# Performance work log

Hardware: AMD Instinct MI355X
Metric: run time of the kernel (lower is better)

Reference implementation:

```python
import jax, jax.numpy as jnp
import numpy as np

N, D = 8192, 256
NUM_CLASSES = 100
WEIGHT = 1.0


def setup_inputs() -> dict:
    key = jax.random.key(0)
    k1, k2 = jax.random.split(key)
    predictions = jax.random.normal(k1, (N, D), dtype=jnp.float32)
    targets = jax.random.randint(k2, (N,), 0, NUM_CLASSES, dtype=jnp.int32)
    return {"predictions": predictions, "targets": targets}


def reference(predictions, targets):
    # Pairwise squared L2 via ||a||^2 + ||b||^2 - 2 a.b  -> [N, N]
    sq = jnp.sum(predictions * predictions, axis=1)
    d2 = sq[:, None] + sq[None, :] - 2.0 * (predictions @ predictions.T)
    dist = jnp.sqrt(jnp.maximum(d2, 0.0))  # torch.dist(p=2)

    n = predictions.shape[0]
    upper = jnp.triu(jnp.ones((n, n), dtype=bool), k=1)  # i < j pairs only
    same = targets[:, None] == targets[None, :]
    mask = upper & same

    num = jnp.sum(mask).astype(dist.dtype)
    loss = jnp.sum(jnp.where(mask, dist, 0.0)) / num
    return loss * WEIGHT
```

## Files before the change

kernel.cpp:

```cpp
#include <hip/hip_runtime.h>

#define N_CLS 100
#define D_DIM 256
#define MAX_M 112
#define ROW_SH 264
#define PANEL 48
#define HALF_R 56

#define AS1 __attribute__((address_space(1)))
#define AS3 __attribute__((address_space(3)))

typedef short bf16x8 __attribute__((ext_vector_type(8)));
typedef float f32x4  __attribute__((ext_vector_type(4)));

__device__ __forceinline__ unsigned short f2bf(float f) {
    unsigned int b = __float_as_uint(f);
    return (unsigned short)((b + 0x7FFFu + ((b >> 16) & 1u)) >> 16);
}

__device__ __forceinline__ void gl_lds16(const void* g, void* l) {
    __builtin_amdgcn_global_load_lds((AS1 void*)g, (AS3 void*)l, 16, 0, 0);
}

__device__ __forceinline__ void stage(const float* __restrict__ pred,
        const int* bkt, int m, int cp0, int dslot, int cnt,
        short* tileS, float* sqs, int wave, int lane) {
    for (int r = wave; r < cnt; r += 8) {
        int cp = cp0 + r;
        float4 v = make_float4(0.f, 0.f, 0.f, 0.f);
        if (cp < m) {
            int g = bkt[cp];
            v = ((const float4*)(pred + (size_t)g * D_DIM))[lane];
        }
        short4 pk;
        pk.x = (short)f2bf(v.x); pk.y = (short)f2bf(v.y);
        pk.z = (short)f2bf(v.z); pk.w = (short)f2bf(v.w);
        *(short4*)&tileS[(dslot + r) * ROW_SH + lane * 4] = pk;
        float s = v.x * v.x + v.y * v.y + v.z * v.z + v.w * v.w;
        #pragma unroll
        for (int o = 32; o; o >>= 1) s += __shfl_xor(s, o, 64);
        if (lane == 0) sqs[dslot + r] = s;
    }
}

__device__ __forceinline__ float tile16(const short* tileS, const float* sqs,
        int a0, int b0, int ga0, int gb0, int m, int lane) {
    const int q = lane >> 4, l15 = lane & 15;
    const short* aP = &tileS[(a0 + l15) * ROW_SH + q * 8];
    const short* bP = &tileS[(b0 + l15) * ROW_SH + q * 8];
    f32x4 acc = {0.f, 0.f, 0.f, 0.f};
    #pragma unroll
    for (int ks = 0; ks < 8; ++ks) {
        bf16x8 af = *(const bf16x8*)(aP + ks * 32);
        bf16x8 bg = *(const bf16x8*)(bP + ks * 32);
        acc = __builtin_amdgcn_mfma_f32_16x16x32_bf16(af, bg, acc, 0, 0, 0);
    }
    float out = 0.f;
    #pragma unroll
    for (int rr = 0; rr < 4; ++rr) {
        int al = q * 4 + rr;
        int pi = ga0 + al, pj = gb0 + l15;
        float d2 = sqs[a0 + al] + sqs[b0 + l15] - 2.f * acc[rr];
        if (pj < m && pi < pj) out += sqrtf(fmaxf(d2, 0.f));
    }
    return out;
}

__global__ __launch_bounds__(512) void k_cls(const float* __restrict__ pred,
        const int* __restrict__ targets, int n, int* __restrict__ bucket_g,
        double* __restrict__ psum, double* __restrict__ pcnt, float* __restrict__ out) {
    __shared__ short tileS[MAX_M * ROW_SH];
    __shared__ __align__(16) float fbuf[HALF_R * D_DIM];
    __shared__ float sqs[MAX_M];
    __shared__ float wsum[8];
    __shared__ int bkt_s[MAX_M];
    __shared__ int cnt_s;
    const int t = threadIdx.x, lane = t & 63, wave = t >> 6;
    const int c = blockIdx.x;
    int* bkt_g = bucket_g + (size_t)c * n;

    if (t == 0) cnt_s = 0;
    __syncthreads();

    if (n == 8192) {
        const int4* tg = (const int4*)targets;
        int4 tv0 = tg[0 * 512 + t], tv1 = tg[1 * 512 + t],
             tv2 = tg[2 * 512 + t], tv3 = tg[3 * 512 + t];
        const int4 tvs[4] = {tv0, tv1, tv2, tv3};
        #pragma unroll
        for (int u = 0; u < 4; ++u) {
            const int base = 4 * (u * 512 + t);
            const int vals[4] = {tvs[u].x, tvs[u].y, tvs[u].z, tvs[u].w};
            #pragma unroll
            for (int e = 0; e < 4; ++e)
                if (vals[e] == c) {
                    int pos = atomicAdd(&cnt_s, 1);
                    if (pos < MAX_M) bkt_s[pos] = base + e;
                    bkt_g[pos] = base + e;
                }
        }
    } else {
        for (int i = t; i < n; i += 512)
            if (targets[i] == c) {
                int pos = atomicAdd(&cnt_s, 1);
                if (pos < MAX_M) bkt_s[pos] = i;
                bkt_g[pos] = i;
            }
    }
    __syncthreads();
    const int m = cnt_s;
    float accum = 0.f;

    if (m <= MAX_M) {
        const int T = (m + 15) >> 4;
        #pragma unroll
        for (int ph = 0; ph < 2; ++ph) {
            const int r0 = ph * HALF_R;
            const int rend = (m < r0 + HALF_R) ? m : (r0 + HALF_R);
            for (int r = r0 + wave; r < rend; r += 8)
                gl_lds16(pred + (size_t)bkt_s[r] * D_DIM + lane * 4,
                         &fbuf[(r - r0) * D_DIM]);
            asm volatile("s_waitcnt vmcnt(0)" ::: "memory");
            for (int r = r0 + wave; r < rend; r += 8) {
                float4 v = *(const float4*)&fbuf[(r - r0) * D_DIM + lane * 4];
                short4 pk;
                pk.x = (short)f2bf(v.x); pk.y = (short)f2bf(v.y);
                pk.z = (short)f2bf(v.z); pk.w = (short)f2bf(v.w);
                *(short4*)&tileS[r * ROW_SH + lane * 4] = pk;
                float s = v.x * v.x + v.y * v.y + v.z * v.z + v.w * v.w;
                #pragma unroll
                for (int o = 32; o; o >>= 1) s += __shfl_xor(s, o, 64);
                if (lane == 0) sqs[r] = s;
            }
            __syncthreads();
        }
        const int np = T * (T + 1) / 2;
        for (int idx = wave; idx < np; idx += 8) {
            int ta = 0, r = idx;
            while (r >= T - ta) { r -= T - ta; ++ta; }
            int tb = ta + r;
            accum += tile16(tileS, sqs, ta * 16, tb * 16, ta * 16, tb * 16, m, lane);
        }
    } else {
        const int P = (m + PANEL - 1) / PANEL;
        for (int pi = 0; pi < P; ++pi)
        for (int pj = pi; pj < P; ++pj) {
            __syncthreads();
            stage(pred, bkt_g, m, pi * PANEL, 0,     PANEL, tileS, sqs, wave, lane);
            stage(pred, bkt_g, m, pj * PANEL, PANEL, PANEL, tileS, sqs, wave, lane);
            __syncthreads();
            for (int idx = wave; idx < 9; idx += 8) {
                int ta = idx / 3, tb = idx % 3;
                accum += tile16(tileS, sqs, ta * 16, PANEL + tb * 16,
                                pi * PANEL + ta * 16, pj * PANEL + tb * 16, m, lane);
            }
        }
    }

    #pragma unroll
    for (int o = 32; o; o >>= 1) accum += __shfl_xor(accum, o, 64);
    if (lane == 0) wsum[wave] = accum;
    __syncthreads();
    if (t == 0) {
        double bs = 0.0;
        #pragma unroll
        for (int w = 0; w < 8; ++w) bs += (double)wsum[w];
        __hip_atomic_store(&psum[c], bs, __ATOMIC_RELAXED, __HIP_MEMORY_SCOPE_AGENT);
        __hip_atomic_store(&pcnt[c], (double)m * (double)(m - 1) * 0.5,
                           __ATOMIC_RELEASE, __HIP_MEMORY_SCOPE_AGENT);
    }

    if (c == 0) {
        double mys = 0.0, myc = 0.0;
        if (t < N_CLS) {
            unsigned long long bits;
            do {
                bits = __hip_atomic_load((const unsigned long long*)&pcnt[t],
                                         __ATOMIC_ACQUIRE, __HIP_MEMORY_SCOPE_AGENT);
            } while (bits >> 63);
            myc = __longlong_as_double((long long)bits);
            unsigned long long sb = __hip_atomic_load((const unsigned long long*)&psum[t],
                                         __ATOMIC_RELAXED, __HIP_MEMORY_SCOPE_AGENT);
            mys = __longlong_as_double((long long)sb);
        }
        __syncthreads();
        double* red_s = (double*)tileS;
        double* red_c = red_s + 128;
        if (t < 128) { red_s[t] = (t < N_CLS) ? mys : 0.0;
                       red_c[t] = (t < N_CLS) ? myc : 0.0; }
        __syncthreads();
        for (int w = 64; w; w >>= 1) {
            if (t < w) { red_s[t] += red_s[t + w]; red_c[t] += red_c[t + w]; }
            __syncthreads();
        }
        if (t == 0) out[0] = (float)(red_c[0] > 0.0 ? red_s[0] / red_c[0] : 0.0);
    }
}

extern "C" void kernel_launch(void* const* d_in, const int* in_sizes, int n_in,
                              void* d_out, int out_size, void* d_ws, size_t ws_size,
                              hipStream_t stream) {
    const float* pred  = (const float*)d_in[0];
    const int* targets = (const int*)d_in[1];
    float* out         = (float*)d_out;
    const int n = in_sizes[1];

    char* ws = (char*)d_ws;
    size_t off = 0;
    double* psum     = (double*)(ws + off); off += N_CLS * 8;
    double* pcnt     = (double*)(ws + off); off += N_CLS * 8;
    int*    bucket_g = (int*)(ws + off);

    k_cls<<<N_CLS, 512, 0, stream>>>(pred, targets, n, bucket_g, psum, pcnt, out);
}
```

Baseline: 68.86 us.

## Replace block-0 spin-wait with last-block reduction and drop redundant bucket stores

The final cross-class reduction no longer makes block 0 spin on every class's count. A global arrival counter now elects the last block to finish, and that block does the reduction, so no block idles waiting for the others. The global bucket index writes are removed from the common small-class path and are only done by a second scan in the rare large-class fallback. The counter assumes the workspace starts at a specific poison value and is reset to it afterwards, which ties correctness to how the harness initialises the workspace.

After: 71.75 us. +4.2%, slower.

```diff
diff --git a/kernel.cpp b/kernel.cpp
--- a/kernel.cpp
+++ b/kernel.cpp
@@ -6,6 +6,7 @@
 #define ROW_SH 264
 #define PANEL 48
 #define HALF_R 56
+#define POISON 0xAAAAAAAAu
 
 #define AS1 __attribute__((address_space(1)))
 #define AS3 __attribute__((address_space(3)))
@@ -68,13 +69,14 @@
 
 __global__ __launch_bounds__(512) void k_cls(const float* __restrict__ pred,
         const int* __restrict__ targets, int n, int* __restrict__ bucket_g,
-        double* __restrict__ psum, double* __restrict__ pcnt, float* __restrict__ out) {
+        double* __restrict__ psum, double* __restrict__ pcnt,
+        unsigned* __restrict__ done, float* __restrict__ out) {
     __shared__ short tileS[MAX_M * ROW_SH];
     __shared__ __align__(16) float fbuf[HALF_R * D_DIM];
     __shared__ float sqs[MAX_M];
     __shared__ float wsum[8];
     __shared__ int bkt_s[MAX_M];
-    __shared__ int cnt_s;
+    __shared__ int cnt_s, cnt2_s, last_s;
     const int t = threadIdx.x, lane = t & 63, wave = t >> 6;
     const int c = blockIdx.x;
     int* bkt_g = bucket_g + (size_t)c * n;
@@ -96,7 +98,6 @@
                 if (vals[e] == c) {
                     int pos = atomicAdd(&cnt_s, 1);
                     if (pos < MAX_M) bkt_s[pos] = base + e;
-                    bkt_g[pos] = base + e;
                 }
         }
     } else {
@@ -104,7 +105,6 @@
             if (targets[i] == c) {
                 int pos = atomicAdd(&cnt_s, 1);
                 if (pos < MAX_M) bkt_s[pos] = i;
-                bkt_g[pos] = i;
             }
     }
     __syncthreads();
@@ -142,6 +142,11 @@
             accum += tile16(tileS, sqs, ta * 16, tb * 16, ta * 16, tb * 16, m, lane);
         }
     } else {
+        if (t == 0) cnt2_s = 0;
+        __syncthreads();
+        for (int i = t; i < n; i += 512)
+            if (targets[i] == c) bkt_g[atomicAdd(&cnt2_s, 1)] = i;
+        __syncthreads();
         const int P = (m + PANEL - 1) / PANEL;
         for (int pi = 0; pi < P; ++pi)
         for (int pj = pi; pj < P; ++pj) {
@@ -167,21 +172,24 @@
         for (int w = 0; w < 8; ++w) bs += (double)wsum[w];
         __hip_atomic_store(&psum[c], bs, __ATOMIC_RELAXED, __HIP_MEMORY_SCOPE_AGENT);
         __hip_atomic_store(&pcnt[c], (double)m * (double)(m - 1) * 0.5,
-                           __ATOMIC_RELEASE, __HIP_MEMORY_SCOPE_AGENT);
-    }
-
-    if (c == 0) {
+                           __ATOMIC_RELAXED, __HIP_MEMORY_SCOPE_AGENT);
+        __threadfence();
+        unsigned old = __hip_atomic_fetch_add(done, 1u, __ATOMIC_ACQ_REL,
+                                              __HIP_MEMORY_SCOPE_AGENT);
+        last_s = (old == POISON + (unsigned)(N_CLS - 1)) ? 1 : 0;
+    }
+    __syncthreads();
+
+    if (last_s) {
+        __threadfence();
         double mys = 0.0, myc = 0.0;
         if (t < N_CLS) {
-            unsigned long long bits;
-            do {
-                bits = __hip_atomic_load((const unsigned long long*)&pcnt[t],
-                                         __ATOMIC_ACQUIRE, __HIP_MEMORY_SCOPE_AGENT);
-            } while (bits >> 63);
-            myc = __longlong_as_double((long long)bits);
             unsigned long long sb = __hip_atomic_load((const unsigned long long*)&psum[t],
                                          __ATOMIC_RELAXED, __HIP_MEMORY_SCOPE_AGENT);
+            unsigned long long cb = __hip_atomic_load((const unsigned long long*)&pcnt[t],
+                                         __ATOMIC_RELAXED, __HIP_MEMORY_SCOPE_AGENT);
             mys = __longlong_as_double((long long)sb);
+            myc = __longlong_as_double((long long)cb);
         }
         __syncthreads();
         double* red_s = (double*)tileS;
@@ -193,7 +201,11 @@
             if (t < w) { red_s[t] += red_s[t + w]; red_c[t] += red_c[t + w]; }
             __syncthreads();
         }
-        if (t == 0) out[0] = (float)(red_c[0] > 0.0 ? red_s[0] / red_c[0] : 0.0);
+        if (t == 0) {
+            out[0] = (float)(red_c[0] > 0.0 ? red_s[0] / red_c[0] : 0.0);
+            __hip_atomic_store(done, POISON, __ATOMIC_RELAXED,
+                               __HIP_MEMORY_SCOPE_AGENT);
+        }
     }
 }
 
@@ -207,9 +219,10 @@
 
     char* ws = (char*)d_ws;
     size_t off = 0;
-    double* psum     = (double*)(ws + off); off += N_CLS * 8;
-    double* pcnt     = (double*)(ws + off); off += N_CLS * 8;
-    int*    bucket_g = (int*)(ws + off);
-
-    k_cls<<<N_CLS, 512, 0, stream>>>(pred, targets, n, bucket_g, psum, pcnt, out);
-}
+    double*   psum = (double*)(ws + off);   off += N_CLS * 8;
+    double*   pcnt = (double*)(ws + off);   off += N_CLS * 8;
+    unsigned* done = (unsigned*)(ws + off); off += 128;
+    int*  bucket_g = (int*)(ws + off);
+
+    k_cls<<<N_CLS, 512, 0, stream>>>(pred, targets, n, bucket_g, psum, pcnt, done, out);
+}
```

## Replace spin-wait final reduction with separate finalize kernel and defer global bucket writes

Applied to the files above, without the earlier changes.

The in-kernel cross-block reduction, where block 0 spin-waited on other blocks' release stores, is replaced by a second tiny kernel launch that sums the per-class partials. Global bucket writes are dropped from the common path and only rebuilt by rescanning targets when a class overflows the shared-memory capacity. This removes the spin-wait, which makes block 0 wait for the slowest block, and it removes scattered global stores. In exchange it adds a kernel launch and a second dependent kernel on the stream.

After: 69.46 us. No clear change (+0.9%).

```diff
diff --git a/kernel.cpp b/kernel.cpp
--- a/kernel.cpp
+++ b/kernel.cpp
@@ -68,13 +68,13 @@
 
 __global__ __launch_bounds__(512) void k_cls(const float* __restrict__ pred,
         const int* __restrict__ targets, int n, int* __restrict__ bucket_g,
-        double* __restrict__ psum, double* __restrict__ pcnt, float* __restrict__ out) {
+        double* __restrict__ psum, double* __restrict__ pcnt) {
     __shared__ short tileS[MAX_M * ROW_SH];
     __shared__ __align__(16) float fbuf[HALF_R * D_DIM];
     __shared__ float sqs[MAX_M];
     __shared__ float wsum[8];
     __shared__ int bkt_s[MAX_M];
-    __shared__ int cnt_s;
+    __shared__ int cnt_s, cnt2_s;
     const int t = threadIdx.x, lane = t & 63, wave = t >> 6;
     const int c = blockIdx.x;
     int* bkt_g = bucket_g + (size_t)c * n;
@@ -96,7 +96,6 @@
                 if (vals[e] == c) {
                     int pos = atomicAdd(&cnt_s, 1);
                     if (pos < MAX_M) bkt_s[pos] = base + e;
-                    bkt_g[pos] = base + e;
                 }
         }
     } else {
@@ -104,7 +103,6 @@
             if (targets[i] == c) {
                 int pos = atomicAdd(&cnt_s, 1);
                 if (pos < MAX_M) bkt_s[pos] = i;
-                bkt_g[pos] = i;
             }
     }
     __syncthreads();
@@ -142,6 +140,11 @@
             accum += tile16(tileS, sqs, ta * 16, tb * 16, ta * 16, tb * 16, m, lane);
         }
     } else {
+        if (t == 0) cnt2_s = 0;
+        __syncthreads();
+        for (int i = t; i < n; i += 512)
+            if (targets[i] == c) bkt_g[atomicAdd(&cnt2_s, 1)] = i;
+        __syncthreads();
         const int P = (m + PANEL - 1) / PANEL;
         for (int pi = 0; pi < P; ++pi)
         for (int pj = pi; pj < P; ++pj) {
@@ -165,36 +168,23 @@
         double bs = 0.0;
         #pragma unroll
         for (int w = 0; w < 8; ++w) bs += (double)wsum[w];
-        __hip_atomic_store(&psum[c], bs, __ATOMIC_RELAXED, __HIP_MEMORY_SCOPE_AGENT);
-        __hip_atomic_store(&pcnt[c], (double)m * (double)(m - 1) * 0.5,
-                           __ATOMIC_RELEASE, __HIP_MEMORY_SCOPE_AGENT);
-    }
-
-    if (c == 0) {
-        double mys = 0.0, myc = 0.0;
-        if (t < N_CLS) {
-            unsigned long long bits;
-            do {
-                bits = __hip_atomic_load((const unsigned long long*)&pcnt[t],
-                                         __ATOMIC_ACQUIRE, __HIP_MEMORY_SCOPE_AGENT);
-            } while (bits >> 63);
-            myc = __longlong_as_double((long long)bits);
-            unsigned long long sb = __hip_atomic_load((const unsigned long long*)&psum[t],
-                                         __ATOMIC_RELAXED, __HIP_MEMORY_SCOPE_AGENT);
-            mys = __longlong_as_double((long long)sb);
-        }
+        psum[c] = bs;
+        pcnt[c] = (double)m * (double)(m - 1) * 0.5;
+    }
+}
+
+__global__ __launch_bounds__(128) void k_fin(const double* __restrict__ psum,
+        const double* __restrict__ pcnt, float* __restrict__ out) {
+    __shared__ double red_s[128], red_c[128];
+    const int t = threadIdx.x;
+    red_s[t] = (t < N_CLS) ? psum[t] : 0.0;
+    red_c[t] = (t < N_CLS) ? pcnt[t] : 0.0;
+    __syncthreads();
+    for (int w = 64; w; w >>= 1) {
+        if (t < w) { red_s[t] += red_s[t + w]; red_c[t] += red_c[t + w]; }
         __syncthreads();
-        double* red_s = (double*)tileS;
-        double* red_c = red_s + 128;
-        if (t < 128) { red_s[t] = (t < N_CLS) ? mys : 0.0;
-                       red_c[t] = (t < N_CLS) ? myc : 0.0; }
-        __syncthreads();
-        for (int w = 64; w; w >>= 1) {
-            if (t < w) { red_s[t] += red_s[t + w]; red_c[t] += red_c[t + w]; }
-            __syncthreads();
-        }
-        if (t == 0) out[0] = (float)(red_c[0] > 0.0 ? red_s[0] / red_c[0] : 0.0);
-    }
+    }
+    if (t == 0) out[0] = (float)(red_c[0] > 0.0 ? red_s[0] / red_c[0] : 0.0);
 }
 
 extern "C" void kernel_launch(void* const* d_in, const int* in_sizes, int n_in,
@@ -211,5 +201,6 @@
     double* pcnt     = (double*)(ws + off); off += N_CLS * 8;
     int*    bucket_g = (int*)(ws + off);
 
-    k_cls<<<N_CLS, 512, 0, stream>>>(pred, targets, n, bucket_g, psum, pcnt, out);
-}
+    k_cls<<<N_CLS, 512, 0, stream>>>(pred, targets, n, bucket_g, psum, pcnt);
+    k_fin<<<1, 128, 0, stream>>>(psum, pcnt, out);
+}
```
